# Kernel tuning notes

Hardware: AMD Instinct MI355X
Metric: run time of the kernel (lower is better)

Reference implementation:

```python
import jax, jax.numpy as jnp
import numpy as np

B, F0, D = 4096, 39, 16
CROSS_LAYER_SIZE = (128, 128)


def _he_uniform(key, shape):
    fan_in = int(np.prod(shape[:-1]))
    limit = np.sqrt(6.0 / fan_in)
    return jax.random.uniform(key, shape, jnp.float32, -limit, limit)


def setup_inputs() -> dict:
    key = jax.random.key(0)
    k_x, k_f0, k_f1, k_w, k_b = jax.random.split(key, 5)
    x = jax.random.normal(k_x, (B, F0, D), dtype=jnp.float32)
    # field_nums with direct=False: [39, 128//2=64, 64]
    f0 = _he_uniform(k_f0, (F0 * F0, CROSS_LAYER_SIZE[0]))          # (1521, 128)
    f1 = _he_uniform(k_f1, (F0 * (CROSS_LAYER_SIZE[0] // 2), CROSS_LAYER_SIZE[1]))  # (2496, 128)
    out_dim = CROSS_LAYER_SIZE[0] // 2 + CROSS_LAYER_SIZE[1]        # 192
    dense_w = _he_uniform(k_w, (out_dim, 1))
    dense_b = jnp.zeros((1,), dtype=jnp.float32)
    return {"x": x, "f0": f0, "f1": f1, "dense_w": dense_w, "dense_b": dense_b}


def reference(x, f0, f1, dense_w, dense_b):
    # CIN forward (direct=False, use_bias=False, use_residual=False, relu)
    # x: (B, F0, D)
    filters = [f0, f1]
    n_layers = len(CROSS_LAYER_SIZE)
    h = x  # hidden state, (B, Fk, D)
    finals = []
    for idx, L in enumerate(CROSS_LAYER_SIZE):
        Fk = h.shape[1]
        # filter f_ has shape (F0*Fk, L) with i (field of x0) major, j (field of h) minor
        Wr = filters[idx].reshape(F0, Fk, L)
        # fused outer product + conv1d (kernel width 1 == matmul over i,j):
        # z[b, m, d] = sum_{i,j} x[b,i,d] * h[b,j,d] * W[i,j,m]
        z = jnp.einsum('bid,bjd,ijm->bmd', x, h, Wr)  # (B, L, D)
        z = jax.nn.relu(z)
        if idx != n_layers - 1:
            # split along feature-map axis: first half feeds next layer,
            # second half goes to output
            h = z[:, : L // 2, :]
            finals.append(z[:, L // 2:, :])
        else:
            finals.append(z)
    result = jnp.sum(jnp.concatenate(finals, axis=1), axis=-1)  # (B, 192)
    return result @ dense_w + dense_b  # (B, 1)
```

## Files before the change

kernel.cpp:

```cpp
#include <hip/hip_runtime.h>


typedef _Float16 h2    __attribute__((ext_vector_type(2)));
typedef _Float16 f16x8 __attribute__((ext_vector_type(8)));
typedef __attribute__((ext_vector_type(16))) float f32x16;

#define XBB 1160

__global__ __launch_bounds__(256)
void CIN_repack(const float* __restrict__ f0, const float* __restrict__ f1,
                uint4* __restrict__ ws)
{
    const int tid  = blockIdx.x * 256 + threadIdx.x;
    const int n    = tid & 127;
    const int slot = tid >> 7;
    const int half = slot & 1;
    const int kh   = (slot >> 1) & 1;
    const int ch   = slot >> 2;
    float v[8];
    if (ch < 50) {
        const int ig = ch / 5, jg = ch - ig * 5;
        const int i = ig * 4 + kh * 2 + half;
        const bool iok = (i < 39);
#pragma unroll
        for (int t = 0; t < 8; ++t) {
            const int j = jg * 8 + t;
            v[t] = (iok && j < 39) ? f0[(i * 39 + j) * 128 + n] : 0.f;
        }
    } else {
        const int c1 = ch - 50;
        const int jg = c1 / 5, ig = c1 - jg * 5;
        const int j = jg * 4 + kh * 2 + half;
#pragma unroll
        for (int t = 0; t < 8; ++t) {
            const int i = ig * 8 + t;
            v[t] = (i < 39) ? f1[(i * 64 + j) * 128 + n] : 0.f;
        }
    }
    union { h2 h[4]; uint4 q; } pk;
#pragma unroll
    for (int t = 0; t < 4; ++t)
        pk.h[t] = h2{(_Float16)v[2 * t], (_Float16)v[2 * t + 1]};
    const int lane = half * 32 + (n & 31);
    const int cg   = n >> 5;
    ws[ch * 512 + kh * 256 + cg * 64 + lane] = pk.q;
}

__global__ __launch_bounds__(256, 2)
void CIN_main(const float* __restrict__ x,
              const char* __restrict__ wsB,
              const float* __restrict__ dw,
              const float* __restrict__ db,
              float* __restrict__ out)
{
    __shared__ __align__(16) _Float16 xsH[8 * XBB];
    __shared__ __align__(4)  _Float16 hsH[8][64][18];
    __shared__ float dws[192];
    __shared__ float red[4][8];

    const int tid  = threadIdx.x;
    const int w    = tid >> 6;
    const int lane = tid & 63;
    const int half = lane >> 5;
    const int d    = lane & 15;
    const int bsel = (lane >> 4) & 1;
    const int col  = lane & 31;

    const char* wbase = wsB + lane * 16 + w * 1024 + 2048;
    f16x8 Bb[2][2];
    auto loadBg = [&](int ch, f16x8 (&B)[2]) {
        const char* p0 = wbase + (size_t)ch * 8192;
        B[0] = *(const f16x8*)(p0 - 2048);
        B[1] = *(const f16x8*)(p0 + 2048);
    };

    loadBg(0, Bb[0]);
    loadBg(1, Bb[1]);

    const float4* xg4 = (const float4*)(x + (size_t)blockIdx.x * 8 * 624);
    for (int e4 = tid; e4 < 1248; e4 += 256) {
        float4 v = xg4[e4];
        int bb = e4 / 156, r = e4 - bb * 156;
        int i = r >> 2, d0 = (r & 3) * 4;
        _Float16* bp = xsH + bb * XBB + i;
        bp[(d0 + 0) * 72] = (_Float16)v.x; bp[(d0 + 1) * 72] = (_Float16)v.y;
        bp[(d0 + 2) * 72] = (_Float16)v.z; bp[(d0 + 3) * 72] = (_Float16)v.w;
    }
    if (tid < 128) { int bb = tid >> 4, dd = tid & 15; xsH[bb * XBB + dd * 72 + 39] = (_Float16)0.f; }
    if (tid < 192) dws[tid] = dw[tid];
    __syncthreads();

    h2 xv[4][20];
#pragma unroll
    for (int p = 0; p < 4; ++p) {
        const uint4* src = (const uint4*)(xsH + (p * 2 + bsel) * XBB + d * 72);
#pragma unroll
        for (int q5 = 0; q5 < 5; ++q5) {
            union { uint4 q; h2 h[4]; } u;
            u.q = src[q5];
#pragma unroll
            for (int t = 0; t < 4; ++t) xv[p][q5 * 4 + t] = u.h[t];
        }
    }

    f32x16 acc[4];
#pragma unroll
    for (int p = 0; p < 4; ++p)
#pragma unroll
        for (int r = 0; r < 16; ++r) acc[p][r] = 0.f;

    h2 xiv2[4][2];

#pragma unroll 1
    for (int o = 0; o < 5; ++o) {
#pragma unroll
        for (int u = 0; u < 10; ++u) {
            const int ch = o * 10 + u;
            const int jg = u % 5;
            if (jg == 0) {
                const int ib = (o * 2 + u / 5) * 4;
#pragma unroll
                for (int p = 0; p < 4; ++p)
#pragma unroll
                    for (int kh = 0; kh < 2; ++kh) {
                        _Float16 s = xsH[(p * 2 + bsel) * XBB + d * 72 + ib + kh * 2 + half];
                        xiv2[p][kh] = h2{s, s};
                    }
            }
#pragma unroll
            for (int p = 0; p < 4; ++p) {
                union { h2 h[4]; f16x8 v; } a0, a1;
#pragma unroll
                for (int q = 0; q < 4; ++q) {
                    a0.h[q] = xiv2[p][0] * xv[p][jg * 4 + q];
                    a1.h[q] = xiv2[p][1] * xv[p][jg * 4 + q];
                }
                acc[p] = __builtin_amdgcn_mfma_f32_32x32x16_f16(a0.v, Bb[u & 1][0], acc[p], 0, 0, 0);
                acc[p] = __builtin_amdgcn_mfma_f32_32x32x16_f16(a1.v, Bb[u & 1][1], acc[p], 0, 0, 0);
            }
            loadBg(ch + 2, Bb[u & 1]);
        }
    }

    float cs[8] = {0.f, 0.f, 0.f, 0.f, 0.f, 0.f, 0.f, 0.f};
    if (w < 2) {
#pragma unroll
        for (int p = 0; p < 4; ++p)
#pragma unroll
            for (int r = 0; r < 16; r += 2) {
                const int row = (r & 3) + 8 * (r >> 2) + 4 * half;
                h2 pr = h2{(_Float16)fmaxf(acc[p][r],     0.f),
                           (_Float16)fmaxf(acc[p][r + 1], 0.f)};
                *(h2*)&hsH[p * 2 + (row >> 4)][w * 32 + col][row & 15] = pr;
            }
    } else {
        const float dwv = dws[(w - 2) * 32 + col];
#pragma unroll
        for (int p = 0; p < 4; ++p)
#pragma unroll
            for (int r = 0; r < 16; ++r) {
                const int row = (r & 3) + 8 * (r >> 2) + 4 * half;
                cs[p * 2 + (row >> 4)] += fmaxf(acc[p][r], 0.f) * dwv;
            }
    }
#pragma unroll
    for (int p = 0; p < 4; ++p)
#pragma unroll
        for (int r = 0; r < 16; ++r) acc[p][r] = 0.f;
    __syncthreads();

#pragma unroll 1
    for (int o2 = 0; o2 < 8; ++o2) {
#pragma unroll
        for (int u = 0; u < 10; ++u) {
            const int ch = 50 + o2 * 10 + u;
            const int ig2 = u % 5;
            if (ig2 == 0) {
                const int jb = (o2 * 2 + u / 5) * 4;
#pragma unroll
                for (int p = 0; p < 4; ++p)
#pragma unroll
                    for (int kh = 0; kh < 2; ++kh) {
                        _Float16 s = hsH[p * 2 + bsel][jb + kh * 2 + half][d];
                        xiv2[p][kh] = h2{s, s};
                    }
            }
#pragma unroll
            for (int p = 0; p < 4; ++p) {
                union { h2 h[4]; f16x8 v; } a0, a1;
#pragma unroll
                for (int q = 0; q < 4; ++q) {
                    a0.h[q] = xiv2[p][0] * xv[p][ig2 * 4 + q];
                    a1.h[q] = xiv2[p][1] * xv[p][ig2 * 4 + q];
                }
                acc[p] = __builtin_amdgcn_mfma_f32_32x32x16_f16(a0.v, Bb[u & 1][0], acc[p], 0, 0, 0);
                acc[p] = __builtin_amdgcn_mfma_f32_32x32x16_f16(a1.v, Bb[u & 1][1], acc[p], 0, 0, 0);
            }
            int chn = ch + 2; if (chn > 129) chn = 129;
            loadBg(chn, Bb[u & 1]);
        }
    }

    {
        const float dwv = dws[64 + w * 32 + col];
#pragma unroll
        for (int p = 0; p < 4; ++p)
#pragma unroll
            for (int r = 0; r < 16; ++r) {
                const int row = (r & 3) + 8 * (r >> 2) + 4 * half;
                cs[p * 2 + (row >> 4)] += fmaxf(acc[p][r], 0.f) * dwv;
            }
    }
#pragma unroll
    for (int rr = 0; rr < 8; ++rr)
#pragma unroll
        for (int off = 32; off > 0; off >>= 1)
            cs[rr] += __shfl_xor(cs[rr], off, 64);
    if (lane == 0) {
#pragma unroll
        for (int rr = 0; rr < 8; ++rr) red[w][rr] = cs[rr];
    }
    __syncthreads();
    if (tid < 8)
        out[blockIdx.x * 8 + tid] = red[0][tid] + red[1][tid] + red[2][tid] + red[3][tid] + db[0];
}

extern "C" void kernel_launch(void* const* d_in, const int* in_sizes, int n_in,
                              void* d_out, int out_size, void* d_ws, size_t ws_size,
                              hipStream_t stream)
{
    const float* x  = (const float*)d_in[0];
    const float* f0 = (const float*)d_in[1];
    const float* f1 = (const float*)d_in[2];
    const float* dw = (const float*)d_in[3];
    const float* db = (const float*)d_in[4];
    float* out = (float*)d_out;

    CIN_repack<<<dim3(260), dim3(256), 0, stream>>>(f0, f1, (uint4*)d_ws);
    CIN_main<<<dim3(512), dim3(256), 0, stream>>>(x, (const char*)d_ws, dw, db, out);
}
```

Measured before the change: 125.1 us.

## Exploit x-x symmetry in layer 0 and halve batch per block

Folds the layer-0 filter symmetrically (W[i,j]+W[j,i] for j>i) during repacking, so only upper-triangular chunks are processed, cutting layer-0 MFMA chunks from 50 to 30. The main kernel now handles 4 batch rows per block with 1024 blocks and a higher occupancy hint, reducing registers and shared memory per block. The trade-off is more total weight streaming per sample and a small fp16 rounding change from summing weights.

```diff
diff --git a/kernel.cpp b/kernel.cpp
--- a/kernel.cpp
+++ b/kernel.cpp
@@ -6,6 +6,13 @@
 typedef __attribute__((ext_vector_type(16))) float f32x16;
 
 #define XBB 1160
+#define L0C 30
+#define NCH 110
+
+__device__ __constant__ int IG0[L0C] = {0,0,0,0,0, 1,1,1,1,1, 2,2,2,2, 3,3,3,3, 4,4,4, 5,5,5, 6,6, 7,7, 8, 9};
+__device__ __constant__ int JG0[L0C] = {0,1,2,3,4, 0,1,2,3,4, 1,2,3,4, 1,2,3,4, 2,3,4, 2,3,4, 3,4, 3,4, 4, 4};
+#define IG0T(c) ((c)<5?0:(c)<10?1:(c)<14?2:(c)<18?3:(c)<21?4:(c)<24?5:(c)<26?6:(c)<28?7:(c)<29?8:9)
+#define JG0T(c) ((c)<10?((c)%5):(c)<18?(((c)-10)%4+1):(c)<24?(((c)-18)%3+2):(c)<28?(((c)-24)%2+3):4)
 
 __global__ __launch_bounds__(256)
 void CIN_repack(const float* __restrict__ f0, const float* __restrict__ f1,
@@ -18,17 +25,21 @@
     const int kh   = (slot >> 1) & 1;
     const int ch   = slot >> 2;
     float v[8];
-    if (ch < 50) {
-        const int ig = ch / 5, jg = ch - ig * 5;
+    if (ch < L0C) {
+        const int ig = IG0[ch], jg = JG0[ch];
         const int i = ig * 4 + kh * 2 + half;
-        const bool iok = (i < 39);
 #pragma unroll
         for (int t = 0; t < 8; ++t) {
             const int j = jg * 8 + t;
-            v[t] = (iok && j < 39) ? f0[(i * 39 + j) * 128 + n] : 0.f;
+            float val = 0.f;
+            if (i < 39 && j < 39 && j >= i) {
+                val = f0[(i * 39 + j) * 128 + n];
+                if (j > i) val += f0[(j * 39 + i) * 128 + n];
+            }
+            v[t] = val;
         }
     } else {
-        const int c1 = ch - 50;
+        const int c1 = ch - L0C;
         const int jg = c1 / 5, ig = c1 - jg * 5;
         const int j = jg * 4 + kh * 2 + half;
 #pragma unroll
@@ -46,17 +57,17 @@
     ws[ch * 512 + kh * 256 + cg * 64 + lane] = pk.q;
 }
 
-__global__ __launch_bounds__(256, 2)
+__global__ __launch_bounds__(256, 4)
 void CIN_main(const float* __restrict__ x,
               const char* __restrict__ wsB,
               const float* __restrict__ dw,
               const float* __restrict__ db,
               float* __restrict__ out)
 {
-    __shared__ __align__(16) _Float16 xsH[8 * XBB];
-    __shared__ __align__(4)  _Float16 hsH[8][64][18];
+    __shared__ __align__(16) _Float16 xsH[4 * XBB];
+    __shared__ __align__(4)  _Float16 hsH[4][64][18];
     __shared__ float dws[192];
-    __shared__ float red[4][8];
+    __shared__ float red[4][4];
 
     const int tid  = threadIdx.x;
     const int w    = tid >> 6;
@@ -77,8 +88,8 @@
     loadBg(0, Bb[0]);
     loadBg(1, Bb[1]);
 
-    const float4* xg4 = (const float4*)(x + (size_t)blockIdx.x * 8 * 624);
-    for (int e4 = tid; e4 < 1248; e4 += 256) {
+    const float4* xg4 = (const float4*)(x + (size_t)blockIdx.x * 4 * 624);
+    for (int e4 = tid; e4 < 624; e4 += 256) {
         float4 v = xg4[e4];
         int bb = e4 / 156, r = e4 - bb * 156;
         int i = r >> 2, d0 = (r & 3) * 4;
@@ -86,13 +97,13 @@
         bp[(d0 + 0) * 72] = (_Float16)v.x; bp[(d0 + 1) * 72] = (_Float16)v.y;
         bp[(d0 + 2) * 72] = (_Float16)v.z; bp[(d0 + 3) * 72] = (_Float16)v.w;
     }
-    if (tid < 128) { int bb = tid >> 4, dd = tid & 15; xsH[bb * XBB + dd * 72 + 39] = (_Float16)0.f; }
+    if (tid < 64) { int bb = tid >> 4, dd = tid & 15; xsH[bb * XBB + dd * 72 + 39] = (_Float16)0.f; }
     if (tid < 192) dws[tid] = dw[tid];
     __syncthreads();
 
-    h2 xv[4][20];
-#pragma unroll
-    for (int p = 0; p < 4; ++p) {
+    h2 xv[2][20];
+#pragma unroll
+    for (int p = 0; p < 2; ++p) {
         const uint4* src = (const uint4*)(xsH + (p * 2 + bsel) * XBB + d * 72);
 #pragma unroll
         for (int q5 = 0; q5 < 5; ++q5) {
@@ -103,49 +114,45 @@
         }
     }
 
-    f32x16 acc[4];
-#pragma unroll
-    for (int p = 0; p < 4; ++p)
+    f32x16 acc[2];
+#pragma unroll
+    for (int p = 0; p < 2; ++p)
 #pragma unroll
         for (int r = 0; r < 16; ++r) acc[p][r] = 0.f;
 
-    h2 xiv2[4][2];
-
-#pragma unroll 1
-    for (int o = 0; o < 5; ++o) {
-#pragma unroll
-        for (int u = 0; u < 10; ++u) {
-            const int ch = o * 10 + u;
-            const int jg = u % 5;
-            if (jg == 0) {
-                const int ib = (o * 2 + u / 5) * 4;
-#pragma unroll
-                for (int p = 0; p < 4; ++p)
-#pragma unroll
-                    for (int kh = 0; kh < 2; ++kh) {
-                        _Float16 s = xsH[(p * 2 + bsel) * XBB + d * 72 + ib + kh * 2 + half];
-                        xiv2[p][kh] = h2{s, s};
-                    }
-            }
-#pragma unroll
-            for (int p = 0; p < 4; ++p) {
-                union { h2 h[4]; f16x8 v; } a0, a1;
-#pragma unroll
-                for (int q = 0; q < 4; ++q) {
-                    a0.h[q] = xiv2[p][0] * xv[p][jg * 4 + q];
-                    a1.h[q] = xiv2[p][1] * xv[p][jg * 4 + q];
+    h2 xiv2[2][2];
+
+#pragma unroll
+    for (int c = 0; c < L0C; ++c) {
+        const int ig = IG0T(c);
+        const int jg = JG0T(c);
+        if (c == 0 || ig != IG0T(c - 1 < 0 ? 0 : c - 1)) {
+#pragma unroll
+            for (int p = 0; p < 2; ++p)
+#pragma unroll
+                for (int kh = 0; kh < 2; ++kh) {
+                    _Float16 s = xsH[(p * 2 + bsel) * XBB + d * 72 + ig * 4 + kh * 2 + half];
+                    xiv2[p][kh] = h2{s, s};
                 }
-                acc[p] = __builtin_amdgcn_mfma_f32_32x32x16_f16(a0.v, Bb[u & 1][0], acc[p], 0, 0, 0);
-                acc[p] = __builtin_amdgcn_mfma_f32_32x32x16_f16(a1.v, Bb[u & 1][1], acc[p], 0, 0, 0);
-            }
-            loadBg(ch + 2, Bb[u & 1]);
-        }
-    }
-
-    float cs[8] = {0.f, 0.f, 0.f, 0.f, 0.f, 0.f, 0.f, 0.f};
+        }
+#pragma unroll
+        for (int p = 0; p < 2; ++p) {
+            union { h2 h[4]; f16x8 v; } a0, a1;
+#pragma unroll
+            for (int q = 0; q < 4; ++q) {
+                a0.h[q] = xiv2[p][0] * xv[p][jg * 4 + q];
+                a1.h[q] = xiv2[p][1] * xv[p][jg * 4 + q];
+            }
+            acc[p] = __builtin_amdgcn_mfma_f32_32x32x16_f16(a0.v, Bb[c & 1][0], acc[p], 0, 0, 0);
+            acc[p] = __builtin_amdgcn_mfma_f32_32x32x16_f16(a1.v, Bb[c & 1][1], acc[p], 0, 0, 0);
+        }
+        loadBg(c + 2, Bb[c & 1]);
+    }
+
+    float cs[4] = {0.f, 0.f, 0.f, 0.f};
     if (w < 2) {
 #pragma unroll
-        for (int p = 0; p < 4; ++p)
+        for (int p = 0; p < 2; ++p)
 #pragma unroll
             for (int r = 0; r < 16; r += 2) {
                 const int row = (r & 3) + 8 * (r >> 2) + 4 * half;
@@ -156,7 +163,7 @@
     } else {
         const float dwv = dws[(w - 2) * 32 + col];
 #pragma unroll
-        for (int p = 0; p < 4; ++p)
+        for (int p = 0; p < 2; ++p)
 #pragma unroll
             for (int r = 0; r < 16; ++r) {
                 const int row = (r & 3) + 8 * (r >> 2) + 4 * half;
@@ -164,7 +171,7 @@
             }
     }
 #pragma unroll
-    for (int p = 0; p < 4; ++p)
+    for (int p = 0; p < 2; ++p)
 #pragma unroll
         for (int r = 0; r < 16; ++r) acc[p][r] = 0.f;
     __syncthreads();
@@ -173,12 +180,12 @@
     for (int o2 = 0; o2 < 8; ++o2) {
 #pragma unroll
         for (int u = 0; u < 10; ++u) {
-            const int ch = 50 + o2 * 10 + u;
+            const int ch = L0C + o2 * 10 + u;
             const int ig2 = u % 5;
             if (ig2 == 0) {
                 const int jb = (o2 * 2 + u / 5) * 4;
 #pragma unroll
-                for (int p = 0; p < 4; ++p)
+                for (int p = 0; p < 2; ++p)
 #pragma unroll
                     for (int kh = 0; kh < 2; ++kh) {
                         _Float16 s = hsH[p * 2 + bsel][jb + kh * 2 + half][d];
@@ -186,7 +193,7 @@
                     }
             }
 #pragma unroll
-            for (int p = 0; p < 4; ++p) {
+            for (int p = 0; p < 2; ++p) {
                 union { h2 h[4]; f16x8 v; } a0, a1;
 #pragma unroll
                 for (int q = 0; q < 4; ++q) {
@@ -196,7 +203,7 @@
                 acc[p] = __builtin_amdgcn_mfma_f32_32x32x16_f16(a0.v, Bb[u & 1][0], acc[p], 0, 0, 0);
                 acc[p] = __builtin_amdgcn_mfma_f32_32x32x16_f16(a1.v, Bb[u & 1][1], acc[p], 0, 0, 0);
             }
-            int chn = ch + 2; if (chn > 129) chn = 129;
+            int chn = ch + 2; if (chn > NCH - 1) chn = NCH - 1;
             loadBg(chn, Bb[u & 1]);
         }
     }
@@ -204,7 +211,7 @@
     {
         const float dwv = dws[64 + w * 32 + col];
 #pragma unroll
-        for (int p = 0; p < 4; ++p)
+        for (int p = 0; p < 2; ++p)
 #pragma unroll
             for (int r = 0; r < 16; ++r) {
                 const int row = (r & 3) + 8 * (r >> 2) + 4 * half;
@@ -212,17 +219,17 @@
             }
     }
 #pragma unroll
-    for (int rr = 0; rr < 8; ++rr)
+    for (int rr = 0; rr < 4; ++rr)
 #pragma unroll
         for (int off = 32; off > 0; off >>= 1)
             cs[rr] += __shfl_xor(cs[rr], off, 64);
     if (lane == 0) {
 #pragma unroll
-        for (int rr = 0; rr < 8; ++rr) red[w][rr] = cs[rr];
+        for (int rr = 0; rr < 4; ++rr) red[w][rr] = cs[rr];
     }
     __syncthreads();
-    if (tid < 8)
-        out[blockIdx.x * 8 + tid] = red[0][tid] + red[1][tid] + red[2][tid] + red[3][tid] + db[0];
+    if (tid < 4)
+        out[blockIdx.x * 4 + tid] = red[0][tid] + red[1][tid] + red[2][tid] + red[3][tid] + db[0];
 }
 
 extern "C" void kernel_launch(void* const* d_in, const int* in_sizes, int n_in,
@@ -236,6 +243,6 @@
     const float* db = (const float*)d_in[4];
     float* out = (float*)d_out;
 
-    CIN_repack<<<dim3(260), dim3(256), 0, stream>>>(f0, f1, (uint4*)d_ws);
-    CIN_main<<<dim3(512), dim3(256), 0, stream>>>(x, (const char*)d_ws, dw, db, out);
+    CIN_repack<<<dim3(220), dim3(256), 0, stream>>>(f0, f1, (uint4*)d_ws);
+    CIN_main<<<dim3(1024), dim3(256), 0, stream>>>(x, (const char*)d_ws, dw, db, out);
 }
```

New measurement: 125.1 us. No clear change (+0.0%).
